# Optimization experiments

Hardware: AMD Instinct MI355X
Metric: run time of the kernel (lower is better)

## Reference

```python
import jax, jax.numpy as jnp
import numpy as np

N_NODES = 100000
N_EDGES = 3200000
N_FEAT = 256
N_FILT = 256


def setup_inputs() -> dict:
    key = jax.random.key(0)
    k1, k2, k3, k4, k5 = jax.random.split(key, 5)
    # Xavier-normal-ish filters: std = sqrt(2/(fan_in+fan_out))
    std = (2.0 / (N_FEAT + N_FILT)) ** 0.5
    filters = jax.random.normal(k1, (N_FEAT, N_FILT), dtype=jnp.float32) * std
    x = jax.random.normal(k2, (N_NODES, N_FEAT), dtype=jnp.float32)
    edge_row = jax.random.randint(k3, (N_EDGES,), 0, N_NODES, dtype=jnp.int32)
    edge_col = jax.random.randint(k4, (N_EDGES,), 0, N_NODES, dtype=jnp.int32)
    edge_weight = jax.random.uniform(k5, (N_EDGES,), dtype=jnp.float32)
    return {"x": x, "filters": filters, "edge_row": edge_row,
            "edge_col": edge_col, "edge_weight": edge_weight}


def reference(x, filters, edge_row, edge_col, edge_weight):
    # XF = x @ filters  -> [N, K]
    XF = jnp.matmul(x, filters)
    # out = transform @ XF, transform given in COO form:
    # out[r] = sum_{e: row[e]==r} weight[e] * XF[col[e]]
    msgs = edge_weight[:, None] * XF[edge_col]          # [E, K] gather
    out = jax.ops.segment_sum(msgs, edge_row, num_segments=N_NODES)  # [N, K] scatter-add
    return out
```

## Files before the change

kernel.cpp:

```cpp
#include <hip/hip_runtime.h>

#define NF 256
#define NK 256
#define NBKT 512
#define TILEA 8192

typedef __attribute__((ext_vector_type(8))) short bf16x8;
typedef __attribute__((ext_vector_type(4))) float f32x4;

__device__ __forceinline__ ushort f2bf(float f) {
  uint u = __float_as_uint(f);
  return (ushort)((u + 0x7fffu + ((u >> 16) & 1u)) >> 16);
}
__device__ __forceinline__ float bf2f(ushort h) {
  return __uint_as_float(((uint)h) << 16);
}

__global__ __launch_bounds__(256) void cvt_filters(const float* __restrict__ F,
                                                   ushort* __restrict__ Ft) {
  int k = blockIdx.x;
  int n = threadIdx.x;
  Ft[(size_t)n * NF + k] = f2bf(F[(size_t)k * NK + n]);
}

__global__ __launch_bounds__(256) void gemm_mfma(const float* __restrict__ x,
                                                 const ushort* __restrict__ Ft,
                                                 ushort* __restrict__ XFh, int M) {
  __shared__ ushort As[16 * NF];
  const int t = threadIdx.x;
  const int row0 = blockIdx.x * 16;

  const float4* xv = (const float4*)(x + (size_t)row0 * NF);
#pragma unroll
  for (int j = 0; j < 4; ++j) {
    int idx = j * 256 + t;
    int r = idx >> 6;
    int c4 = idx & 63;
    float4 v = make_float4(0.f, 0.f, 0.f, 0.f);
    if (row0 + r < M) v = xv[idx];
    ushort4 h = make_ushort4(f2bf(v.x), f2bf(v.y), f2bf(v.z), f2bf(v.w));
    uint boff = (uint)(r * 512 + c4 * 8);
    boff ^= (uint)((r & 7) << 4);
    *(ushort4*)((char*)As + boff) = h;
  }
  __syncthreads();

  const int lane = t & 63;
  const int wv = t >> 6;
  const int arow = lane & 15;
  const int kg = lane >> 4;

  bf16x8 afr[8];
#pragma unroll
  for (int kk = 0; kk < 8; ++kk) {
    uint boff = (uint)(arow * 512 + kk * 64 + kg * 16);
    boff ^= (uint)((arow & 7) << 4);
    afr[kk] = *(const bf16x8*)((const char*)As + boff);
  }

  f32x4 acc[4];
#pragma unroll
  for (int f = 0; f < 4; ++f) acc[f] = (f32x4){0.f, 0.f, 0.f, 0.f};

  const int ncol0 = wv * 64;
#pragma unroll
  for (int f = 0; f < 4; ++f) {
    const ushort* bp = Ft + (size_t)(ncol0 + f * 16 + arow) * NF + kg * 8;
#pragma unroll
    for (int kk = 0; kk < 8; ++kk) {
      bf16x8 bfr = *(const bf16x8*)(bp + kk * 32);
      acc[f] = __builtin_amdgcn_mfma_f32_16x16x32_bf16(afr[kk], bfr, acc[f], 0, 0, 0);
    }
  }

#pragma unroll
  for (int f = 0; f < 4; ++f) {
    int col = ncol0 + f * 16 + arow;
#pragma unroll
    for (int rg = 0; rg < 4; ++rg) {
      int row = row0 + kg * 4 + rg;
      if (row < M) XFh[(size_t)row * NK + col] = f2bf(acc[f][rg]);
    }
  }
}

__global__ __launch_bounds__(256) void coarse_hist(const int* __restrict__ erow,
                                                   int* __restrict__ bcnt, int nE) {
  __shared__ int h[NBKT];
  h[threadIdx.x] = 0;
  h[threadIdx.x + 256] = 0;
  __syncthreads();
  for (int e = blockIdx.x * 256 + threadIdx.x; e < nE; e += gridDim.x * 256)
    atomicAdd(&h[erow[e] >> 8], 1);
  __syncthreads();
  int v0 = h[threadIdx.x], v1 = h[threadIdx.x + 256];
  if (v0) atomicAdd(&bcnt[threadIdx.x], v0);
  if (v1) atomicAdd(&bcnt[threadIdx.x + 256], v1);
}

__global__ __launch_bounds__(512) void scan_bbase(const int* __restrict__ bcnt,
                                                  int* __restrict__ bbase,
                                                  int* __restrict__ bcursor) {
  __shared__ int s[NBKT];
  int t = threadIdx.x;
  int v = bcnt[t];
  s[t] = v;
  __syncthreads();
  for (int d = 1; d < NBKT; d <<= 1) {
    int tmp = (t >= d) ? s[t - d] : 0;
    __syncthreads();
    s[t] += tmp;
    __syncthreads();
  }
  int excl = s[t] - v;
  bbase[t] = excl;
  bcursor[t * 16] = excl;
}

__global__ __launch_bounds__(512) void bin_coarse(const int* __restrict__ erow,
                                                  const int* __restrict__ ecol,
                                                  const float* __restrict__ ew,
                                                  int* __restrict__ bcursor,
                                                  int2* __restrict__ tmpCW, int nE) {
  __shared__ int h[NBKT];
  __shared__ int lb[NBKT];
  __shared__ int gb[NBKT];
  __shared__ int2 pay[TILEA];
  const int t = threadIdx.x;
  const int base = blockIdx.x * TILEA;

  h[t] = 0;
  __syncthreads();

  int rnk[16], bb[16], loc[16];
#pragma unroll
  for (int k = 0; k < 16; ++k) {
    int i = base + k * 512 + t;
    rnk[k] = -1; bb[k] = 0; loc[k] = 0;
    if (i < nE) {
      int row = erow[i];
      bb[k] = row >> 8;
      loc[k] = row & 255;
      rnk[k] = atomicAdd(&h[bb[k]], 1);
    }
  }
  __syncthreads();

  int hv = h[t];
  lb[t] = hv;
  __syncthreads();
  for (int d = 1; d < NBKT; d <<= 1) {
    int tmp = (t >= d) ? lb[t - d] : 0;
    __syncthreads();
    lb[t] += tmp;
    __syncthreads();
  }
  int ex = lb[t] - hv;
  __syncthreads();
  lb[t] = ex;
  if (hv > 0) gb[t] = atomicAdd(&bcursor[t * 16], hv);
  __syncthreads();

#pragma unroll
  for (int k = 0; k < 16; ++k) {
    int i = base + k * 512 + t;
    if (i < nE) {
      int pos = lb[bb[k]] + rnk[k];
      pay[pos] = make_int2(ecol[i] | (loc[k] << 20), __float_as_int(ew[i]));
    }
  }
  __syncthreads();

  const int wv = t >> 6, lane = t & 63;
  for (int b = wv; b < NBKT; b += 8) {
    int len = h[b];
    if (!len) continue;
    int lbase = lb[b], gbase = gb[b];
    for (int off = lane; off < len; off += 64)
      tmpCW[gbase + off] = pay[lbase + off];
  }
}

__global__ __launch_bounds__(256) void bin_fine(const int2* __restrict__ tmpCW,
                                                const int* __restrict__ bbase,
                                                const int* __restrict__ bcnt,
                                                int* __restrict__ offsets,
                                                int2* __restrict__ cw,
                                                int nNodes, int nE) {
  __shared__ int hist[256];
  __shared__ int cur[256];
  const int b = blockIdx.x;
  const int t = threadIdx.x;
  const int base = bbase[b];
  const int n = bcnt[b];

  hist[t] = 0;
  __syncthreads();
  for (int i = t; i < n; i += 256)
    atomicAdd(&hist[((uint)tmpCW[base + i].x) >> 20], 1);
  __syncthreads();

  int hv = hist[t];
  cur[t] = hv;
  __syncthreads();
  for (int d = 1; d < 256; d <<= 1) {
    int tmp = (t >= d) ? cur[t - d] : 0;
    __syncthreads();
    cur[t] += tmp;
    __syncthreads();
  }
  int ex = cur[t] - hv;
  __syncthreads();
  cur[t] = ex;
  int node = (b << 8) + t;
  if (node < nNodes) offsets[node] = base + ex;
  if (b == 0 && t == 0) offsets[nNodes] = nE;
  __syncthreads();

  for (int i = t; i < n; i += 256) {
    int2 v = tmpCW[base + i];
    int local = ((uint)v.x) >> 20;
    int d = base + atomicAdd(&cur[local], 1);
    cw[d] = make_int2(v.x & 0xFFFFF, v.y);
  }
}

__global__ __launch_bounds__(256) void gather_bf16(const ushort* __restrict__ XFh,
                                                   const int* __restrict__ offsets,
                                                   const int2* __restrict__ cw,
                                                   float4* __restrict__ outv,
                                                   int nNodes) {
  const int lane = threadIdx.x & 63;
  const int node = (blockIdx.x * blockDim.x + threadIdx.x) >> 6;
  if (node >= nNodes) return;
  const int start = offsets[node];
  const int end = offsets[node + 1];
  const ushort4* XV = (const ushort4*)XFh;

  float ax = 0.f, ay = 0.f, az = 0.f, aw = 0.f;
  for (int base = start; base < end; base += 64) {
    int n = end - base;
    if (n > 64) n = 64;
    int2 e = make_int2(0, 0);
    if (lane < n) e = cw[base + lane];
    int j = 0;
    for (; j + 3 < n; j += 4) {
      int c0 = __shfl(e.x, j),     c1 = __shfl(e.x, j + 1);
      int c2 = __shfl(e.x, j + 2), c3 = __shfl(e.x, j + 3);
      float w0 = __int_as_float(__shfl(e.y, j));
      float w1 = __int_as_float(__shfl(e.y, j + 1));
      float w2 = __int_as_float(__shfl(e.y, j + 2));
      float w3 = __int_as_float(__shfl(e.y, j + 3));
      ushort4 v0 = XV[(size_t)c0 * 64 + lane];
      ushort4 v1 = XV[(size_t)c1 * 64 + lane];
      ushort4 v2 = XV[(size_t)c2 * 64 + lane];
      ushort4 v3 = XV[(size_t)c3 * 64 + lane];
      ax += w0 * bf2f(v0.x); ay += w0 * bf2f(v0.y); az += w0 * bf2f(v0.z); aw += w0 * bf2f(v0.w);
      ax += w1 * bf2f(v1.x); ay += w1 * bf2f(v1.y); az += w1 * bf2f(v1.z); aw += w1 * bf2f(v1.w);
      ax += w2 * bf2f(v2.x); ay += w2 * bf2f(v2.y); az += w2 * bf2f(v2.z); aw += w2 * bf2f(v2.w);
      ax += w3 * bf2f(v3.x); ay += w3 * bf2f(v3.y); az += w3 * bf2f(v3.z); aw += w3 * bf2f(v3.w);
    }
    for (; j < n; ++j) {
      int c0 = __shfl(e.x, j);
      float w0 = __int_as_float(__shfl(e.y, j));
      ushort4 v0 = XV[(size_t)c0 * 64 + lane];
      ax += w0 * bf2f(v0.x); ay += w0 * bf2f(v0.y); az += w0 * bf2f(v0.z); aw += w0 * bf2f(v0.w);
    }
  }
  outv[(size_t)node * 64 + lane] = make_float4(ax, ay, az, aw);
}

__global__ __launch_bounds__(256) void gemm_xf(const float* __restrict__ x,
                                               const float* __restrict__ F,
                                               float* __restrict__ XF, int M) {
  __shared__ float xs[64][NF];
  const int t = threadIdx.x;
  const int row0 = blockIdx.x * 64;
  const int rows = min(64, M - row0);
  const float4* xv = (const float4*)(x + (size_t)row0 * NF);
  float4* xsv = (float4*)&xs[0][0];
#pragma unroll
  for (int j = 0; j < 16; ++j) {
    int i = j * 256 + t;
    int r = i >> 6;
    float4 v;
    if (r < rows) v = xv[i];
    else          v = make_float4(0.f, 0.f, 0.f, 0.f);
    xsv[i] = v;
  }
  __syncthreads();
  const int r0 = (t >> 5) * 8;
  const int c0 = blockIdx.y * 128 + (t & 31) * 4;
  float acc[8][4];
#pragma unroll
  for (int r = 0; r < 8; ++r)
#pragma unroll
    for (int c = 0; c < 4; ++c) acc[r][c] = 0.f;
  for (int k = 0; k < NF; k += 4) {
    float4 f0 = *(const float4*)(F + (size_t)(k + 0) * NK + c0);
    float4 f1 = *(const float4*)(F + (size_t)(k + 1) * NK + c0);
    float4 f2 = *(const float4*)(F + (size_t)(k + 2) * NK + c0);
    float4 f3 = *(const float4*)(F + (size_t)(k + 3) * NK + c0);
#pragma unroll
    for (int r = 0; r < 8; ++r) {
      float4 xr = *(const float4*)&xs[r0 + r][k];
      acc[r][0] += xr.x * f0.x + xr.y * f1.x + xr.z * f2.x + xr.w * f3.x;
      acc[r][1] += xr.x * f0.y + xr.y * f1.y + xr.z * f2.y + xr.w * f3.y;
      acc[r][2] += xr.x * f0.z + xr.y * f1.z + xr.z * f2.z + xr.w * f3.z;
      acc[r][3] += xr.x * f0.w + xr.y * f1.w + xr.z * f2.w + xr.w * f3.w;
    }
  }
#pragma unroll
  for (int r = 0; r < 8; ++r) {
    int row = r0 + r;
    if (row < rows) {
      float4 v = make_float4(acc[r][0], acc[r][1], acc[r][2], acc[r][3]);
      *(float4*)(XF + (size_t)(row0 + row) * NK + c0) = v;
    }
  }
}

__global__ __launch_bounds__(256) void scatter_edges(
    const float* __restrict__ XF, const int* __restrict__ erow,
    const int* __restrict__ ecol, const float* __restrict__ ew,
    float* __restrict__ out, int nE) {
  const int lane = threadIdx.x & 63;
  const int wid = (blockIdx.x * blockDim.x + threadIdx.x) >> 6;
  const int nwaves = (gridDim.x * blockDim.x) >> 6;
  for (int e = wid; e < nE; e += nwaves) {
    const int r = erow[e];
    const int c = ecol[e];
    const float w = ew[e];
    float4 v = *(const float4*)(XF + (size_t)c * NK + lane * 4);
    float* dst = out + (size_t)r * NK + lane * 4;
    atomicAdd(dst + 0, w * v.x);
    atomicAdd(dst + 1, w * v.y);
    atomicAdd(dst + 2, w * v.z);
    atomicAdd(dst + 3, w * v.w);
  }
}

static inline size_t align16(size_t x) { return (x + 15) & ~(size_t)15; }

extern "C" void kernel_launch(void* const* d_in, const int* in_sizes, int n_in,
                              void* d_out, int out_size, void* d_ws, size_t ws_size,
                              hipStream_t stream) {
  const float* x  = (const float*)d_in[0];
  const float* F  = (const float*)d_in[1];
  const int* erow = (const int*)d_in[2];
  const int* ecol = (const int*)d_in[3];
  const float* ew = (const float*)d_in[4];
  float* out      = (float*)d_out;

  const int M      = in_sizes[0] / NF;
  const int nE     = in_sizes[2];
  const int nNodes = out_size / NK;

  char* base = (char*)d_ws;
  size_t off = 0;
  ushort* XFh  = (ushort*)(base + off); off += align16((size_t)M * NK * sizeof(ushort));
  ushort* Ft   = (ushort*)(base + off); off += align16((size_t)NF * NK * sizeof(ushort));
  int* offsets = (int*)(base + off);    off += align16(((size_t)nNodes + 1) * sizeof(int));
  int* bcnt    = (int*)(base + off);    off += align16(NBKT * sizeof(int));
  int* bbase   = (int*)(base + off);    off += align16(NBKT * sizeof(int));
  int* bcursor = (int*)(base + off);    off += align16((size_t)NBKT * 16 * sizeof(int));
  int2* tmpCW  = (int2*)(base + off);   off += align16((size_t)nE * sizeof(int2));
  int2* cw     = (int2*)(base + off);   off += align16((size_t)nE * sizeof(int2));
  const size_t needed = off;

  const int nb2 = (nNodes + 255) >> 8;
  const bool ok = (ws_size >= needed) && (nb2 <= NBKT) &&
                  (nNodes < (1 << 20)) && (M < (1 << 20));

  if (ok) {
    cvt_filters<<<NF, NK, 0, stream>>>(F, Ft);
    gemm_mfma<<<(M + 15) / 16, 256, 0, stream>>>(x, Ft, XFh, M);
    hipMemsetAsync(bcnt, 0, NBKT * sizeof(int), stream);
    coarse_hist<<<2048, 256, 0, stream>>>(erow, bcnt, nE);
    scan_bbase<<<1, NBKT, 0, stream>>>(bcnt, bbase, bcursor);
    bin_coarse<<<(nE + TILEA - 1) / TILEA, 512, 0, stream>>>(erow, ecol, ew,
                                                             bcursor, tmpCW, nE);
    bin_fine<<<nb2, 256, 0, stream>>>(tmpCW, bbase, bcnt, offsets, cw, nNodes, nE);
    int gblocks = (nNodes + 3) / 4;
    gather_bf16<<<gblocks, 256, 0, stream>>>(XFh, offsets, cw, (float4*)out, nNodes);
  } else {
    float* XF = (float*)d_ws;
    dim3 gg((M + 63) / 64, NK / 128);
    gemm_xf<<<gg, 256, 0, stream>>>(x, F, XF, M);
    hipMemsetAsync(d_out, 0, (size_t)out_size * sizeof(float), stream);
    scatter_edges<<<2048, 256, 0, stream>>>(XF, erow, ecol, ew, out, nE);
  }
}
```

Baseline: 474.9 us.

## Fuse filter convert with histogram, widen GEMM tile, unroll gather, nontemporal IO

Merges the filter transpose/convert kernel and the coarse edge histogram into one launch, so one kernel launch goes away. Doubles the GEMM row tile to 32 rows per block so each B fragment feeds two MFMAs, which halves filter loads per output. Adds an 8-way unrolled gather loop for more memory-level parallelism. Uses nontemporal loads for edge records and nontemporal stores for the output. The larger GEMM tile raises register and LDS use and may lower occupancy.

```diff
diff --git a/kernel.cpp b/kernel.cpp
--- a/kernel.cpp
+++ b/kernel.cpp
@@ -16,32 +16,49 @@
   return __uint_as_float(((uint)h) << 16);
 }
 
-__global__ __launch_bounds__(256) void cvt_filters(const float* __restrict__ F,
-                                                   ushort* __restrict__ Ft) {
-  int k = blockIdx.x;
-  int n = threadIdx.x;
-  Ft[(size_t)n * NF + k] = f2bf(F[(size_t)k * NK + n]);
+__global__ __launch_bounds__(256) void prelude(const float* __restrict__ F,
+                                               ushort* __restrict__ Ft,
+                                               const int* __restrict__ erow,
+                                               int* __restrict__ bcnt, int nE) {
+  __shared__ int h[NBKT];
+  if (blockIdx.x < NF) {
+    int k = blockIdx.x;
+    int n = threadIdx.x;
+    Ft[(size_t)n * NF + k] = f2bf(F[(size_t)k * NK + n]);
+    return;
+  }
+  const int bid = blockIdx.x - NF;
+  const int nb = gridDim.x - NF;
+  h[threadIdx.x] = 0;
+  h[threadIdx.x + 256] = 0;
+  __syncthreads();
+  for (int e = bid * 256 + threadIdx.x; e < nE; e += nb * 256)
+    atomicAdd(&h[erow[e] >> 8], 1);
+  __syncthreads();
+  int v0 = h[threadIdx.x], v1 = h[threadIdx.x + 256];
+  if (v0) atomicAdd(&bcnt[threadIdx.x], v0);
+  if (v1) atomicAdd(&bcnt[threadIdx.x + 256], v1);
 }
 
 __global__ __launch_bounds__(256) void gemm_mfma(const float* __restrict__ x,
                                                  const ushort* __restrict__ Ft,
                                                  ushort* __restrict__ XFh, int M) {
-  __shared__ ushort As[16 * NF];
+  __shared__ ushort As[32 * NF];
   const int t = threadIdx.x;
-  const int row0 = blockIdx.x * 16;
+  const int row0 = blockIdx.x * 32;
 
   const float4* xv = (const float4*)(x + (size_t)row0 * NF);
 #pragma unroll
-  for (int j = 0; j < 4; ++j) {
+  for (int j = 0; j < 8; ++j) {
     int idx = j * 256 + t;
     int r = idx >> 6;
     int c4 = idx & 63;
     float4 v = make_float4(0.f, 0.f, 0.f, 0.f);
     if (row0 + r < M) v = xv[idx];
-    ushort4 h = make_ushort4(f2bf(v.x), f2bf(v.y), f2bf(v.z), f2bf(v.w));
+    ushort4 hh = make_ushort4(f2bf(v.x), f2bf(v.y), f2bf(v.z), f2bf(v.w));
     uint boff = (uint)(r * 512 + c4 * 8);
     boff ^= (uint)((r & 7) << 4);
-    *(ushort4*)((char*)As + boff) = h;
+    *(ushort4*)((char*)As + boff) = hh;
   }
   __syncthreads();
 
@@ -50,17 +67,23 @@
   const int arow = lane & 15;
   const int kg = lane >> 4;
 
-  bf16x8 afr[8];
-#pragma unroll
-  for (int kk = 0; kk < 8; ++kk) {
-    uint boff = (uint)(arow * 512 + kk * 64 + kg * 16);
-    boff ^= (uint)((arow & 7) << 4);
-    afr[kk] = *(const bf16x8*)((const char*)As + boff);
-  }
-
-  f32x4 acc[4];
-#pragma unroll
-  for (int f = 0; f < 4; ++f) acc[f] = (f32x4){0.f, 0.f, 0.f, 0.f};
+  bf16x8 afr[2][8];
+#pragma unroll
+  for (int rt = 0; rt < 2; ++rt) {
+#pragma unroll
+    for (int kk = 0; kk < 8; ++kk) {
+      int r = rt * 16 + arow;
+      uint boff = (uint)(r * 512 + kk * 64 + kg * 16);
+      boff ^= (uint)((r & 7) << 4);
+      afr[rt][kk] = *(const bf16x8*)((const char*)As + boff);
+    }
+  }
+
+  f32x4 acc[2][4];
+#pragma unroll
+  for (int rt = 0; rt < 2; ++rt)
+#pragma unroll
+    for (int f = 0; f < 4; ++f) acc[rt][f] = (f32x4){0.f, 0.f, 0.f, 0.f};
 
   const int ncol0 = wv * 64;
 #pragma unroll
@@ -69,33 +92,23 @@
 #pragma unroll
     for (int kk = 0; kk < 8; ++kk) {
       bf16x8 bfr = *(const bf16x8*)(bp + kk * 32);
-      acc[f] = __builtin_amdgcn_mfma_f32_16x16x32_bf16(afr[kk], bfr, acc[f], 0, 0, 0);
-    }
-  }
-
-#pragma unroll
-  for (int f = 0; f < 4; ++f) {
-    int col = ncol0 + f * 16 + arow;
-#pragma unroll
-    for (int rg = 0; rg < 4; ++rg) {
-      int row = row0 + kg * 4 + rg;
-      if (row < M) XFh[(size_t)row * NK + col] = f2bf(acc[f][rg]);
-    }
-  }
-}
-
-__global__ __launch_bounds__(256) void coarse_hist(const int* __restrict__ erow,
-                                                   int* __restrict__ bcnt, int nE) {
-  __shared__ int h[NBKT];
-  h[threadIdx.x] = 0;
-  h[threadIdx.x + 256] = 0;
-  __syncthreads();
-  for (int e = blockIdx.x * 256 + threadIdx.x; e < nE; e += gridDim.x * 256)
-    atomicAdd(&h[erow[e] >> 8], 1);
-  __syncthreads();
-  int v0 = h[threadIdx.x], v1 = h[threadIdx.x + 256];
-  if (v0) atomicAdd(&bcnt[threadIdx.x], v0);
-  if (v1) atomicAdd(&bcnt[threadIdx.x + 256], v1);
+      acc[0][f] = __builtin_amdgcn_mfma_f32_16x16x32_bf16(afr[0][kk], bfr, acc[0][f], 0, 0, 0);
+      acc[1][f] = __builtin_amdgcn_mfma_f32_16x16x32_bf16(afr[1][kk], bfr, acc[1][f], 0, 0, 0);
+    }
+  }
+
+#pragma unroll
+  for (int rt = 0; rt < 2; ++rt) {
+#pragma unroll
+    for (int f = 0; f < 4; ++f) {
+      int col = ncol0 + f * 16 + arow;
+#pragma unroll
+      for (int rg = 0; rg < 4; ++rg) {
+        int row = row0 + rt * 16 + kg * 4 + rg;
+        if (row < M) XFh[(size_t)row * NK + col] = f2bf(acc[rt][f][rg]);
+      }
+    }
+  }
 }
 
 __global__ __launch_bounds__(512) void scan_bbase(const int* __restrict__ bcnt,
@@ -228,7 +241,7 @@
 __global__ __launch_bounds__(256) void gather_bf16(const ushort* __restrict__ XFh,
                                                    const int* __restrict__ offsets,
                                                    const int2* __restrict__ cw,
-                                                   float4* __restrict__ outv,
+                                                   f32x4* __restrict__ outv,
                                                    int nNodes) {
   const int lane = threadIdx.x & 63;
   const int node = (blockIdx.x * blockDim.x + threadIdx.x) >> 6;
@@ -242,8 +255,42 @@
     int n = end - base;
     if (n > 64) n = 64;
     int2 e = make_int2(0, 0);
-    if (lane < n) e = cw[base + lane];
+    if (lane < n) {
+      long long raw = __builtin_nontemporal_load((const long long*)(cw + base + lane));
+      e.x = (int)(raw & 0xFFFFFFFFll);
+      e.y = (int)(raw >> 32);
+    }
     int j = 0;
+    for (; j + 7 < n; j += 8) {
+      int c0 = __shfl(e.x, j),     c1 = __shfl(e.x, j + 1);
+      int c2 = __shfl(e.x, j + 2), c3 = __shfl(e.x, j + 3);
+      int c4 = __shfl(e.x, j + 4), c5 = __shfl(e.x, j + 5);
+      int c6 = __shfl(e.x, j + 6), c7 = __shfl(e.x, j + 7);
+      float w0 = __int_as_float(__shfl(e.y, j));
+      float w1 = __int_as_float(__shfl(e.y, j + 1));
+      float w2 = __int_as_float(__shfl(e.y, j + 2));
+      float w3 = __int_as_float(__shfl(e.y, j + 3));
+      float w4 = __int_as_float(__shfl(e.y, j + 4));
+      float w5 = __int_as_float(__shfl(e.y, j + 5));
+      float w6 = __int_as_float(__shfl(e.y, j + 6));
+      float w7 = __int_as_float(__shfl(e.y, j + 7));
+      ushort4 v0 = XV[(size_t)c0 * 64 + lane];
+      ushort4 v1 = XV[(size_t)c1 * 64 + lane];
+      ushort4 v2 = XV[(size_t)c2 * 64 + lane];
+      ushort4 v3 = XV[(size_t)c3 * 64 + lane];
+      ushort4 v4 = XV[(size_t)c4 * 64 + lane];
+      ushort4 v5 = XV[(size_t)c5 * 64 + lane];
+      ushort4 v6 = XV[(size_t)c6 * 64 + lane];
+      ushort4 v7 = XV[(size_t)c7 * 64 + lane];
+      ax += w0 * bf2f(v0.x); ay += w0 * bf2f(v0.y); az += w0 * bf2f(v0.z); aw += w0 * bf2f(v0.w);
+      ax += w1 * bf2f(v1.x); ay += w1 * bf2f(v1.y); az += w1 * bf2f(v1.z); aw += w1 * bf2f(v1.w);
+      ax += w2 * bf2f(v2.x); ay += w2 * bf2f(v2.y); az += w2 * bf2f(v2.z); aw += w2 * bf2f(v2.w);
+      ax += w3 * bf2f(v3.x); ay += w3 * bf2f(v3.y); az += w3 * bf2f(v3.z); aw += w3 * bf2f(v3.w);
+      ax += w4 * bf2f(v4.x); ay += w4 * bf2f(v4.y); az += w4 * bf2f(v4.z); aw += w4 * bf2f(v4.w);
+      ax += w5 * bf2f(v5.x); ay += w5 * bf2f(v5.y); az += w5 * bf2f(v5.z); aw += w5 * bf2f(v5.w);
+      ax += w6 * bf2f(v6.x); ay += w6 * bf2f(v6.y); az += w6 * bf2f(v6.z); aw += w6 * bf2f(v6.w);
+      ax += w7 * bf2f(v7.x); ay += w7 * bf2f(v7.y); az += w7 * bf2f(v7.z); aw += w7 * bf2f(v7.w);
+    }
     for (; j + 3 < n; j += 4) {
       int c0 = __shfl(e.x, j),     c1 = __shfl(e.x, j + 1);
       int c2 = __shfl(e.x, j + 2), c3 = __shfl(e.x, j + 3);
@@ -267,7 +314,8 @@
       ax += w0 * bf2f(v0.x); ay += w0 * bf2f(v0.y); az += w0 * bf2f(v0.z); aw += w0 * bf2f(v0.w);
     }
   }
-  outv[(size_t)node * 64 + lane] = make_float4(ax, ay, az, aw);
+  f32x4 r; r.x = ax; r.y = ay; r.z = az; r.w = aw;
+  __builtin_nontemporal_store(r, &outv[(size_t)node * 64 + lane]);
 }
 
 __global__ __launch_bounds__(256) void gemm_xf(const float* __restrict__ x,
@@ -373,16 +421,15 @@
                   (nNodes < (1 << 20)) && (M < (1 << 20));
 
   if (ok) {
-    cvt_filters<<<NF, NK, 0, stream>>>(F, Ft);
-    gemm_mfma<<<(M + 15) / 16, 256, 0, stream>>>(x, Ft, XFh, M);
     hipMemsetAsync(bcnt, 0, NBKT * sizeof(int), stream);
-    coarse_hist<<<2048, 256, 0, stream>>>(erow, bcnt, nE);
+    prelude<<<NF + 2048, 256, 0, stream>>>(F, Ft, erow, bcnt, nE);
+    gemm_mfma<<<(M + 31) / 32, 256, 0, stream>>>(x, Ft, XFh, M);
     scan_bbase<<<1, NBKT, 0, stream>>>(bcnt, bbase, bcursor);
     bin_coarse<<<(nE + TILEA - 1) / TILEA, 512, 0, stream>>>(erow, ecol, ew,
                                                              bcursor, tmpCW, nE);
     bin_fine<<<nb2, 256, 0, stream>>>(tmpCW, bbase, bcnt, offsets, cw, nNodes, nE);
     int gblocks = (nNodes + 3) / 4;
-    gather_bf16<<<gblocks, 256, 0, stream>>>(XFh, offsets, cw, (float4*)out, nNodes);
+    gather_bf16<<<gblocks, 256, 0, stream>>>(XFh, offsets, cw, (f32x4*)out, nNodes);
   } else {
     float* XF = (float*)d_ws;
     dim3 gg((M + 63) / 64, NK / 128);
```

After: 432.5 us. 8.9% less time.
